# Kernel tuning notes

Measured on AMD Instinct MI355X. Metric: run time of the kernel, lower is better.

Reference implementation:

```python
import jax, jax.numpy as jnp
import numpy as np

EPS_DIST = 1e-10
BN_EPS = 1e-5
K = 3  # nsample / three_nn


def setup_inputs() -> dict:
    key = jax.random.key(0)
    ks = jax.random.split(key, 8)
    B, N, S, D1, D2 = 4, 8192, 2048, 128, 256
    C_in = D1 + D2  # 384
    H = 256
    inp = {
        "pos1": jax.random.normal(ks[0], (B, 3, N), dtype=jnp.float32),
        "pos2": jax.random.normal(ks[1], (B, 3, S), dtype=jnp.float32),
        "feature1": jax.random.normal(ks[2], (B, D1, N), dtype=jnp.float32),
        "feature2": jax.random.normal(ks[3], (B, D2, S), dtype=jnp.float32),
        # MLP layer 1: Conv1d(384->256, k=1) + BN
        "W1": jax.random.normal(ks[4], (H, C_in), dtype=jnp.float32) * (1.0 / np.sqrt(C_in)),
        "b1": jnp.zeros((H,), dtype=jnp.float32),
        "g1": jnp.ones((H,), dtype=jnp.float32),
        "be1": jnp.zeros((H,), dtype=jnp.float32),
        # MLP layer 2: Conv1d(256->256, k=1) + BN
        "W2": jax.random.normal(ks[5], (H, H), dtype=jnp.float32) * (1.0 / np.sqrt(H)),
        "b2": jnp.zeros((H,), dtype=jnp.float32),
        "g2": jnp.ones((H,), dtype=jnp.float32),
        "be2": jnp.zeros((H,), dtype=jnp.float32),
    }
    return inp


def _conv_bn_relu(x, W, b, gamma, beta):
    # x: [B, Cin, N]; 1x1 Conv1d == channel GEMM
    y = jnp.einsum("oc,bcn->bon", W, x) + b[None, :, None]
    # BatchNorm1d in training mode: batch statistics over (B, N)
    mean = jnp.mean(y, axis=(0, 2), keepdims=True)
    var = jnp.mean(jnp.square(y - mean), axis=(0, 2), keepdims=True)
    y = (y - mean) * jax.lax.rsqrt(var + BN_EPS)
    y = y * gamma[None, :, None] + beta[None, :, None]
    return jax.nn.relu(y)


def reference(pos1, pos2, feature1, feature2, W1, b1, g1, be1, W2, b2, g2, be2):
    # pos1: [B,3,N], pos2: [B,3,S], feature1: [B,D1,N], feature2: [B,D2,S]
    p1 = jnp.swapaxes(pos1, 1, 2)  # [B,N,3]
    p2 = jnp.swapaxes(pos2, 1, 2)  # [B,S,3]
    # three_nn: squared-distance 3-NN of each point in p1 among p2
    d2 = (jnp.sum(p1 * p1, -1)[:, :, None]
          + jnp.sum(p2 * p2, -1)[:, None, :]
          - 2.0 * jnp.einsum("bnc,bsc->bns", p1, p2))  # [B,N,S]
    neg_vals, idx = jax.lax.top_k(-d2, K)  # idx: [B,N,3]
    dists = jnp.maximum(-neg_vals, EPS_DIST)  # dists[dists<1e-10]=1e-10
    w = 1.0 / dists
    w = w / jnp.sum(w, -1, keepdims=True)  # [B,N,3]
    # grouping_operation: gather feature2 [B,D,S] by idx -> [B,D,N,3]
    grouped = jax.vmap(lambda f, i: f[:, i])(feature2, idx)
    interpolated = jnp.sum(grouped * w[:, None, :, :], axis=-1)  # [B,D2,N]
    feat = jnp.concatenate([interpolated, feature1], axis=1)  # [B,384,N]
    feat = _conv_bn_relu(feat, W1, b1, g1, be1)
    feat = _conv_bn_relu(feat, W2, b2, g2, be2)
    return feat  # [B,256,N]
```

## Files before the change

### kernel.cpp

```cpp
#include <hip/hip_runtime.h>
#include <hip/hip_bf16.h>
#include <cstdint>

typedef unsigned short u16;
typedef unsigned int u32;
typedef unsigned long long u64;
typedef __bf16 bf16x8 __attribute__((ext_vector_type(8)));
typedef float f32x4 __attribute__((ext_vector_type(4)));
typedef u16 u16x8 __attribute__((ext_vector_type(8)));

#define FPSCALE 1048576.0f
#define FPINV   (1.0f / 1048576.0f)
#define NSLICE 16

__device__ __forceinline__ u16 f2b(float f) {
    unsigned int u = __float_as_uint(f);
    u += 0x7fffu + ((u >> 16) & 1u);
    return (u16)(u >> 16);
}
__device__ __forceinline__ float b2f(u16 h) {
    return __uint_as_float(((unsigned int)h) << 16);
}
__device__ __forceinline__ void async_cp16(void* lds, const void* g) {
    __builtin_amdgcn_global_load_lds((const __attribute__((address_space(1))) void*)g,
                                     (__attribute__((address_space(3))) void*)lds, 16, 0, 0);
}
__device__ __forceinline__ u64 ld_agent_u64(const u64* p) {
    return __hip_atomic_load(p, __ATOMIC_RELAXED, __HIP_MEMORY_SCOPE_AGENT);
}
__device__ __forceinline__ u32 fmono(float f) {
    u32 u = __float_as_uint(f);
    return u ^ (((u32)((int)u >> 31)) | 0x80000000u);
}
__device__ __forceinline__ u64 shfl_xor_u64(u64 v, int mask) {
    u32 lo = (u32)v, hi = (u32)(v >> 32);
    lo = (u32)__shfl_xor((int)lo, mask);
    hi = (u32)__shfl_xor((int)hi, mask);
    return ((u64)hi << 32) | lo;
}
__device__ __forceinline__ void ins3(u64 k, u64& k0, u64& k1, u64& k2) {
    bool c0 = k > k0, c1 = k > k1, c2 = k > k2;
    k2 = c1 ? k1 : (c2 ? k : k2);
    k1 = c0 ? k0 : (c1 ? k : k1);
    k0 = c0 ? k : k0;
}
__device__ __forceinline__ int pkix(int i) { return i + (i >> 6); }

#define NB_NN  2048
#define NB_CVT 160
#define NB_T2  512
#define NB_T1  1024

__global__ __launch_bounds__(256, 8) void prep_kernel(const float* __restrict__ w1,
                                                      const float* __restrict__ w2,
                                                      u16* __restrict__ wb,
                                                      const float* __restrict__ feature2,
                                                      u16* __restrict__ f2t,
                                                      const float* __restrict__ feature1,
                                                      u16* __restrict__ f1t,
                                                      const float* __restrict__ pos1,
                                                      const float* __restrict__ pos2,
                                                      int* __restrict__ idx_out,
                                                      float* __restrict__ w_out,
                                                      u64* __restrict__ SZ) {
    __shared__ __align__(16) char smem[18176];
    int bi = blockIdx.x;
    int tid = threadIdx.x;

    if (bi >= NB_NN) {
        int ci = bi - NB_NN;
        if (ci >= NB_CVT + NB_T2 + NB_T1) {
            for (int i = tid; i < 2 * NSLICE * 512; i += 256) SZ[i] = 0;
            if (tid == 0) *(int*)(SZ + 2 * NSLICE * 512) = 0;
            return;
        }
        if (ci < NB_CVT) {
            int i = ci * 256 + tid;
            if (i < 40960) {
                const float* src = (i < 24576) ? w1 : w2;
                int k = (i < 24576) ? i : (i - 24576);
                float4 v = *(const float4*)&src[(size_t)k * 4];
                ushort4 o;
                o.x = f2b(v.x); o.y = f2b(v.y); o.z = f2b(v.z); o.w = f2b(v.w);
                *(ushort4*)&wb[(size_t)i * 4] = o;
            }
            return;
        }
        float (*t)[65] = (float (*)[65])smem;
        const float* in; u16* out; int C, S, s0, c0, b;
        if (ci < NB_CVT + NB_T2) {
            int lin = ci - NB_CVT;
            C = 256; S = 2048; in = feature2; out = f2t;
            s0 = (lin & 31) * 64; c0 = ((lin >> 5) & 3) * 64; b = lin >> 7;
        } else {
            int lin = ci - NB_CVT - NB_T2;
            C = 128; S = 8192; in = feature1; out = f1t;
            s0 = (lin & 127) * 64; c0 = ((lin >> 7) & 1) * 64; b = lin >> 8;
        }
        const float* ib = in + (size_t)b * C * S;
        u16* ob = out + (size_t)b * S * C;
        int col = tid & 63, r0 = tid >> 6;
#pragma unroll
        for (int p = 0; p < 16; ++p) {
            int c = p * 4 + r0;
            t[c][col] = ib[(size_t)(c0 + c) * S + s0 + col];
        }
        __syncthreads();
#pragma unroll
        for (int p = 0; p < 16; ++p) {
            int s = p * 4 + r0;
            ob[(size_t)(s0 + s) * C + c0 + col] = f2b(t[col][s]);
        }
        return;
    }

    float4* pk = (float4*)smem;
    u64* warr = (u64*)(smem + 16640);
    int j0 = bi * 16;
    int b = j0 >> 13;
    const float* p2 = pos2 + (size_t)b * 3 * 2048;
    int p = tid & 15, ck = tid >> 4;
    int wv = tid >> 6, lane = tid & 63;
    const float* p1 = pos1 + (size_t)b * 3 * 8192;
    int n = (j0 & 8191) + p;
    float qx = p1[n], qy = p1[8192 + n], qz = p1[16384 + n];
    u64 key0 = 0, key1 = 0, key2 = 0;

    for (int half = 0; half < 2; ++half) {
        int hbase = half * 1024;
        for (int i = tid; i < 1024; i += 256) {
            int s = hbase + i;
            float x = p2[s], y = p2[2048 + s], z = p2[4096 + s];
            pk[pkix(i)] = make_float4(x, y, z, -0.5f * (x * x + y * y + z * z));
        }
        __syncthreads();

        float g0 = -3.4e38f, g1 = -3.4e38f, g2 = -3.4e38f;
        int id0 = 0, id1 = 0, id2 = 0;
        int sb = ck * 64;
        const float4* pc = pk + pkix(sb);
#pragma unroll 4
        for (int it = 0; it < 64; ++it) {
            float4 cd = pc[it];
            int s = sb + it;
            float tv = fmaf(qx, cd.x, fmaf(qy, cd.y, fmaf(qz, cd.z, cd.w)));
            bool c0 = tv > g0, c1 = tv > g1, c2 = tv > g2;
            float o0 = g0, o1 = g1;
            g2 = __builtin_amdgcn_fmed3f(tv, o1, g2);
            g1 = __builtin_amdgcn_fmed3f(tv, o0, o1);
            g0 = fmaxf(o0, tv);
            id2 = c1 ? id1 : (c2 ? s : id2);
            id1 = c0 ? id0 : (c1 ? s : id1);
            id0 = c0 ? s : id0;
        }
        __syncthreads();

        ins3(((u64)fmono(g0) << 32) | (u64)(2047 - (hbase + id0)), key0, key1, key2);
        ins3(((u64)fmono(g1) << 32) | (u64)(2047 - (hbase + id1)), key0, key1, key2);
        ins3(((u64)fmono(g2) << 32) | (u64)(2047 - (hbase + id2)), key0, key1, key2);
    }

#pragma unroll
    for (int mask = 16; mask <= 32; mask <<= 1) {
        u64 m0 = shfl_xor_u64(key0, mask);
        u64 m1 = shfl_xor_u64(key1, mask);
        u64 m2 = shfl_xor_u64(key2, mask);
        ins3(m0, key0, key1, key2);
        ins3(m1, key0, key1, key2);
        ins3(m2, key0, key1, key2);
    }
    if (lane < 16) {
        u64* wr = &warr[(wv * 16 + p) * 3];
        wr[0] = key0; wr[1] = key1; wr[2] = key2;
    }
    __syncthreads();
    if (tid < 16) {
        int pp = tid;
        const u64* w0 = &warr[pp * 3];
        u64 k0 = w0[0], k1 = w0[1], k2 = w0[2];
#pragma unroll
        for (int w = 1; w < 4; ++w) {
            const u64* wr = &warr[(w * 16 + pp) * 3];
            ins3(wr[0], k0, k1, k2);
            ins3(wr[1], k0, k1, k2);
            ins3(wr[2], k0, k1, k2);
        }
        int s0 = 2047 - (int)(k0 & 0xFFFFFFFFu);
        int s1 = 2047 - (int)(k1 & 0xFFFFFFFFu);
        int s2 = 2047 - (int)(k2 & 0xFFFFFFFFu);
        int j = j0 + pp;
        int nn = j & 8191;
        float x1 = p1[nn], y1 = p1[8192 + nn], z1 = p1[16384 + nn];
        float n1 = x1 * x1 + y1 * y1 + z1 * z1;
        float X0 = p2[s0], Y0 = p2[2048 + s0], Z0 = p2[4096 + s0];
        float X1 = p2[s1], Y1v = p2[2048 + s1], Z1 = p2[4096 + s1];
        float X2 = p2[s2], Y2v = p2[2048 + s2], Z2 = p2[4096 + s2];
        float t0 = x1 * X0 + y1 * Y0 + z1 * Z0 - 0.5f * (X0 * X0 + Y0 * Y0 + Z0 * Z0);
        float t1 = x1 * X1 + y1 * Y1v + z1 * Z1 - 0.5f * (X1 * X1 + Y1v * Y1v + Z1 * Z1);
        float t2 = x1 * X2 + y1 * Y2v + z1 * Z2 - 0.5f * (X2 * X2 + Y2v * Y2v + Z2 * Z2);
        float d0 = fmaxf(fmaf(-2.f, t0, n1), 1e-10f);
        float d1 = fmaxf(fmaf(-2.f, t1, n1), 1e-10f);
        float d2 = fmaxf(fmaf(-2.f, t2, n1), 1e-10f);
        float w0v = 1.f / d0, w1v = 1.f / d1, w2v = 1.f / d2;
        float inv = 1.f / (w0v + w1v + w2v);
        idx_out[j * 3] = s0; idx_out[j * 3 + 1] = s1; idx_out[j * 3 + 2] = s2;
        w_out[j * 3] = w0v * inv; w_out[j * 3 + 1] = w1v * inv; w_out[j * 3 + 2] = w2v * inv;
    }
}

__global__ __launch_bounds__(256, 8) void interp_kernel(const u16* __restrict__ f2t,
                                                        const int* __restrict__ idx,
                                                        const float* __restrict__ wgt,
                                                        u16* __restrict__ out) {
    int tid = threadIdx.x;
    int j = blockIdx.x * 16 + (tid >> 4);
    int c0 = (tid & 15) * 16;
    int b = j >> 13;
    const u16* fb = f2t + (size_t)b * 2048 * 256;
    const u16* r0 = fb + (size_t)idx[j * 3 + 0] * 256 + c0;
    const u16* r1 = fb + (size_t)idx[j * 3 + 1] * 256 + c0;
    const u16* r2 = fb + (size_t)idx[j * 3 + 2] * 256 + c0;
    float w0 = wgt[j * 3 + 0], w1 = wgt[j * 3 + 1], w2 = wgt[j * 3 + 2];
    u16* ob = out + (size_t)j * 256 + c0;
#pragma unroll
    for (int cc = 0; cc < 2; ++cc) {
        u16x8 v0 = *(const u16x8*)(r0 + cc * 8);
        u16x8 v1 = *(const u16x8*)(r1 + cc * 8);
        u16x8 v2 = *(const u16x8*)(r2 + cc * 8);
        u16x8 o;
#pragma unroll
        for (int e = 0; e < 8; ++e)
            o[e] = f2b(w0 * b2f(v0[e]) + w1 * b2f(v1[e]) + w2 * b2f(v2[e]));
        *(u16x8*)(ob + cc * 8) = o;
    }
}

__device__ __forceinline__ void gridbar(int* cnt, int target) {
    __syncthreads();
    if (threadIdx.x == 0) {
        __hip_atomic_fetch_add(cnt, 1, __ATOMIC_RELAXED, __HIP_MEMORY_SCOPE_AGENT);
        while (__hip_atomic_load(cnt, __ATOMIC_RELAXED, __HIP_MEMORY_SCOPE_AGENT) < target)
            __builtin_amdgcn_s_sleep(16);
        __atomic_signal_fence(__ATOMIC_SEQ_CST);
    }
    __syncthreads();
}

__global__ __launch_bounds__(256, 1) void mlp_fused(const u16* __restrict__ A1,
                                                    const u16* __restrict__ A2g,
                                                    const u16* __restrict__ W1b,
                                                    const float* __restrict__ b1,
                                                    const u16* __restrict__ W2b,
                                                    const float* __restrict__ b2,
                                                    u64* __restrict__ S1,
                                                    const float* __restrict__ g1,
                                                    const float* __restrict__ be1,
                                                    u64* __restrict__ S2,
                                                    const float* __restrict__ g2,
                                                    const float* __restrict__ be2,
                                                    float* __restrict__ OUT,
                                                    int* __restrict__ BAR) {
    __shared__ __align__(16) char smem[98304];
    u16* AS  = (u16*)smem;
    u16* BS  = (u16*)(smem + 16384);
    u16* A2  = (u16*)smem;
    u16* BS2 = (u16*)(smem + 65536);
    float* SC  = (float*)(smem + 65536);
    float* SC2 = (float*)(smem + 65536 + 4096);
    float2* BNT = (float2*)(smem + 65536);

    int tid = threadIdx.x, bid = blockIdx.x;
    int lane = tid & 63, wv = tid >> 6;
    int l15 = lane & 15, q = lane >> 4;
    int lrow = lane >> 3, lchunk = lane & 7, schunk = lchunk ^ lrow;
    int j0 = bid * 128;
    int wrow = wv * 32;
    int sl = (bid & (NSLICE - 1)) * 512;

    f32x4 acc[2][16];
#pragma unroll
    for (int i = 0; i < 2; ++i)
#pragma unroll
        for (int jj = 0; jj < 16; ++jj) acc[i][jj] = (f32x4){0.f, 0.f, 0.f, 0.f};

    for (int k0 = 0; k0 < 384; k0 += 64) {
#pragma unroll
        for (int qq = 0; qq < 8; ++qq) {
            int row = wv * 64 + qq * 8;
            async_cp16(&BS[row * 64], W1b + (size_t)(row + lrow) * 384 + k0 + schunk * 8);
        }
        const u16* src; int str;
        if (k0 < 256) { src = A1 + (size_t)j0 * 256 + k0;          str = 256; }
        else          { src = A2g + (size_t)j0 * 128 + (k0 - 256); str = 128; }
#pragma unroll
        for (int qq = 0; qq < 4; ++qq) {
            int row = wv * 32 + qq * 8;
            async_cp16(&AS[row * 64], src + (size_t)(row + lrow) * str + schunk * 8);
        }
        __syncthreads();
#pragma unroll
        for (int ks = 0; ks < 2; ++ks) {
            bf16x8 af[2];
#pragma unroll
            for (int i = 0; i < 2; ++i) {
                int row = wrow + i * 16 + l15;
                af[i] = *(const bf16x8*)&AS[row * 64 + ((ks * 4 + q) ^ (l15 & 7)) * 8];
            }
#pragma unroll
            for (int jj = 0; jj < 16; ++jj) {
                int row = jj * 16 + l15;
                bf16x8 bfr = *(const bf16x8*)&BS[row * 64 + ((ks * 4 + q) ^ (l15 & 7)) * 8];
#pragma unroll
                for (int i = 0; i < 2; ++i)
                    acc[i][jj] = __builtin_amdgcn_mfma_f32_16x16x32_bf16(af[i], bfr,
                                                                         acc[i][jj], 0, 0, 0);
            }
        }
        __syncthreads();
    }

#pragma unroll
    for (int jj = 0; jj < 16; ++jj) {
        float bv = b1[jj * 16 + l15];
        float s = 0.f, s2 = 0.f;
#pragma unroll
        for (int i = 0; i < 2; ++i)
#pragma unroll
            for (int r = 0; r < 4; ++r) {
                acc[i][jj][r] += bv;
                float v = acc[i][jj][r];
                s += v; s2 += v * v;
            }
        s += __shfl_xor(s, 16); s += __shfl_xor(s, 32);
        s2 += __shfl_xor(s2, 16); s2 += __shfl_xor(s2, 32);
        if (q == 0) {
            SC[wv * 256 + jj * 16 + l15] = s;
            SC2[wv * 256 + jj * 16 + l15] = s2;
        }
    }
    __syncthreads();
    {
        float fs = SC[tid] + SC[256 + tid] + SC[512 + tid] + SC[768 + tid];
        float fs2 = SC2[tid] + SC2[256 + tid] + SC2[512 + tid] + SC2[768 + tid];
        atomicAdd(&S1[sl + tid], (u64)(long long)llrintf(fs * FPSCALE));
        atomicAdd(&S1[sl + 256 + tid], (u64)(long long)llrintf(fs2 * FPSCALE));
    }
    gridbar(BAR, 256);

    {
        long long su = 0, sq = 0;
#pragma unroll
        for (int r = 0; r < NSLICE; ++r) {
            su += (long long)ld_agent_u64(&S1[r * 512 + tid]);
            sq += (long long)ld_agent_u64(&S1[r * 512 + 256 + tid]);
        }
        float fs = (float)su * FPINV;
        float fs2 = (float)sq * FPINV;
        const float inv = 1.f / 32768.f;
        float mean = fs * inv;
        float var = fs2 * inv - mean * mean;
        float a = g1[tid] * rsqrtf(var + 1e-5f);
        BNT[tid] = make_float2(a, be1[tid] - mean * a);
    }
    __syncthreads();

#pragma unroll
    for (int i = 0; i < 2; ++i)
#pragma unroll
        for (int jj = 0; jj < 16; ++jj) {
            int c = jj * 16 + l15;
            float2 bn = BNT[c];
            int chunkbase = c >> 3;
            int win = c & 7;
#pragma unroll
            for (int r = 0; r < 4; ++r) {
                int row = wrow + i * 16 + q * 4 + r;
                float vb = b2f(f2b(acc[i][jj][r]));
                u16 h = f2b(fmaxf(vb * bn.x + bn.y, 0.f));
                A2[row * 256 + ((chunkbase ^ (row & 7)) * 8 + win)] = h;
            }
        }
    __syncthreads();

#pragma unroll
    for (int i = 0; i < 2; ++i)
#pragma unroll
        for (int jj = 0; jj < 16; ++jj) acc[i][jj] = (f32x4){0.f, 0.f, 0.f, 0.f};

    for (int kstep = 0; kstep < 4; ++kstep) {
        int k0 = kstep * 64;
#pragma unroll
        for (int qq = 0; qq < 8; ++qq) {
            int row = wv * 64 + qq * 8;
            async_cp16(&BS2[row * 64], W2b + (size_t)(row + lrow) * 256 + k0 + schunk * 8);
        }
        __syncthreads();
#pragma unroll
        for (int ks = 0; ks < 2; ++ks) {
            bf16x8 af[2];
#pragma unroll
            for (int i = 0; i < 2; ++i) {
                int row = wrow + i * 16 + l15;
                int kc = kstep * 8 + ks * 4 + q;
                af[i] = *(const bf16x8*)&A2[row * 256 + ((kc ^ (row & 7)) * 8)];
            }
#pragma unroll
            for (int jj = 0; jj < 16; ++jj) {
                int row = jj * 16 + l15;
                bf16x8 bfr = *(const bf16x8*)&BS2[row * 64 + ((ks * 4 + q) ^ (l15 & 7)) * 8];
#pragma unroll
                for (int i = 0; i < 2; ++i)
                    acc[i][jj] = __builtin_amdgcn_mfma_f32_16x16x32_bf16(af[i], bfr,
                                                                         acc[i][jj], 0, 0, 0);
            }
        }
        __syncthreads();
    }

#pragma unroll
    for (int jj = 0; jj < 16; ++jj) {
        float bv = b2[jj * 16 + l15];
        float s = 0.f, s2 = 0.f;
#pragma unroll
        for (int i = 0; i < 2; ++i)
#pragma unroll
            for (int r = 0; r < 4; ++r) {
                acc[i][jj][r] += bv;
                float v = acc[i][jj][r];
                s += v; s2 += v * v;
            }
        s += __shfl_xor(s, 16); s += __shfl_xor(s, 32);
        s2 += __shfl_xor(s2, 16); s2 += __shfl_xor(s2, 32);
        if (q == 0) {
            SC[wv * 256 + jj * 16 + l15] = s;
            SC2[wv * 256 + jj * 16 + l15] = s2;
        }
    }
    __syncthreads();
    {
        float fs = SC[tid] + SC[256 + tid] + SC[512 + tid] + SC[768 + tid];
        float fs2 = SC2[tid] + SC2[256 + tid] + SC2[512 + tid] + SC2[768 + tid];
        atomicAdd(&S2[sl + tid], (u64)(long long)llrintf(fs * FPSCALE));
        atomicAdd(&S2[sl + 256 + tid], (u64)(long long)llrintf(fs2 * FPSCALE));
    }
    gridbar(BAR, 512);

    {
        long long su = 0, sq = 0;
#pragma unroll
        for (int r = 0; r < NSLICE; ++r) {
            su += (long long)ld_agent_u64(&S2[r * 512 + tid]);
            sq += (long long)ld_agent_u64(&S2[r * 512 + 256 + tid]);
        }
        float fs = (float)su * FPINV;
        float fs2 = (float)sq * FPINV;
        const float inv = 1.f / 32768.f;
        float mean = fs * inv;
        float var = fs2 * inv - mean * mean;
        float a = g2[tid] * rsqrtf(var + 1e-5f);
        BNT[tid] = make_float2(a, be2[tid] - mean * a);
    }
    __syncthreads();

    int bb = j0 >> 13, nbase = j0 & 8191;
#pragma unroll
    for (int i = 0; i < 2; ++i)
#pragma unroll
        for (int jj = 0; jj < 16; ++jj) {
            int o = jj * 16 + l15;
            float2 bn = BNT[o];
            int n0 = nbase + wrow + i * 16 + q * 4;
            float4 v;
            v.x = fmaxf(b2f(f2b(acc[i][jj][0])) * bn.x + bn.y, 0.f);
            v.y = fmaxf(b2f(f2b(acc[i][jj][1])) * bn.x + bn.y, 0.f);
            v.z = fmaxf(b2f(f2b(acc[i][jj][2])) * bn.x + bn.y, 0.f);
            v.w = fmaxf(b2f(f2b(acc[i][jj][3])) * bn.x + bn.y, 0.f);
            *(float4*)&OUT[(size_t)bb * 2097152 + (size_t)o * 8192 + n0] = v;
        }
}

extern "C" void kernel_launch(void* const* d_in, const int* in_sizes, int n_in,
                              void* d_out, int out_size, void* d_ws, size_t ws_size,
                              hipStream_t stream) {
    const float* pos1 = (const float*)d_in[0];
    const float* pos2 = (const float*)d_in[1];
    const float* feature1 = (const float*)d_in[2];
    const float* feature2 = (const float*)d_in[3];
    const float* W1 = (const float*)d_in[4];
    const float* b1 = (const float*)d_in[5];
    const float* g1 = (const float*)d_in[6];
    const float* be1 = (const float*)d_in[7];
    const float* W2 = (const float*)d_in[8];
    const float* b2 = (const float*)d_in[9];
    const float* g2 = (const float*)d_in[10];
    const float* be2 = (const float*)d_in[11];

    char* ws = (char*)d_ws;
    int*    IDX   = (int*)(ws + 0);
    float*  WGT   = (float*)(ws + 393216);
    u16*    W1B   = (u16*)(ws + 786432);
    u16*    W2B   = (u16*)(ws + 983040);
    u16*    F2T   = (u16*)(ws + 1118208);
    u16*    F1T   = (u16*)(ws + 5312512);
    u16*    INTERP= (u16*)(ws + 30478336);
    u64*    SSTAT = (u64*)(ws + 47255552);
    u64*    S1    = SSTAT;
    u64*    S2    = SSTAT + NSLICE * 512;
    int*    BAR   = (int*)(SSTAT + 2 * NSLICE * 512);
    float*  OUT   = (float*)d_out;

    prep_kernel<<<NB_NN + NB_CVT + NB_T2 + NB_T1 + 1, 256, 0, stream>>>(
        W1, W2, W1B, feature2, F2T, feature1, F1T, pos1, pos2, IDX, WGT, SSTAT);
    interp_kernel<<<2048, 256, 0, stream>>>(F2T, IDX, WGT, INTERP);
    mlp_fused<<<256, 256, 0, stream>>>(INTERP, F1T, W1B, b1, W2B, b2,
                                       S1, g1, be1, S2, g2, be2, OUT, BAR);
}
```

Before: 183.2 us.

## Double-buffer MLP GEMM loads and split output channels across 8 waves

The fused MLP kernel now runs 512 threads per block, with waves split into 4 row groups and 2 column groups so each wave holds half as many accumulators. Both GEMM phases get double-buffered LDS staging, so the next K-slice of weights and activations is prefetched while the current one is computed. The first W2 slice is also prefetched before the BN1 grid barrier. The aim is to hide global-to-LDS latency and gain more latency hiding from extra waves per CU. The cost is more shared memory (about 138 KB) and a larger block.

```diff
diff --git a/kernel.cpp b/kernel.cpp
--- a/kernel.cpp
+++ b/kernel.cpp
@@ -246,7 +246,7 @@
     __syncthreads();
 }
 
-__global__ __launch_bounds__(256, 1) void mlp_fused(const u16* __restrict__ A1,
+__global__ __launch_bounds__(512, 1) void mlp_fused(const u16* __restrict__ A1,
                                                     const u16* __restrict__ A2g,
                                                     const u16* __restrict__ W1b,
                                                     const float* __restrict__ b1,
@@ -260,56 +260,79 @@
                                                     const float* __restrict__ be2,
                                                     float* __restrict__ OUT,
                                                     int* __restrict__ BAR) {
-    __shared__ __align__(16) char smem[98304];
+    __shared__ __align__(16) char smem[141312];
     u16* AS  = (u16*)smem;
-    u16* BS  = (u16*)(smem + 16384);
+    u16* BS  = (u16*)(smem + 32768);
     u16* A2  = (u16*)smem;
     u16* BS2 = (u16*)(smem + 65536);
-    float* SC  = (float*)(smem + 65536);
-    float* SC2 = (float*)(smem + 65536 + 4096);
-    float2* BNT = (float2*)(smem + 65536);
+    float* SC  = (float*)(smem + 131072);
+    float* SC2 = (float*)(smem + 135168);
+    float2* BNT = (float2*)(smem + 139264);
 
     int tid = threadIdx.x, bid = blockIdx.x;
     int lane = tid & 63, wv = tid >> 6;
     int l15 = lane & 15, q = lane >> 4;
     int lrow = lane >> 3, lchunk = lane & 7, schunk = lchunk ^ lrow;
     int j0 = bid * 128;
-    int wrow = wv * 32;
+    int rw = wv & 3;
+    int cg = wv >> 2;
+    int wrow = rw * 32;
+    int cbase = cg * 128;
     int sl = (bid & (NSLICE - 1)) * 512;
 
-    f32x4 acc[2][16];
+    f32x4 acc[2][8];
 #pragma unroll
     for (int i = 0; i < 2; ++i)
 #pragma unroll
-        for (int jj = 0; jj < 16; ++jj) acc[i][jj] = (f32x4){0.f, 0.f, 0.f, 0.f};
-
-    for (int k0 = 0; k0 < 384; k0 += 64) {
-#pragma unroll
-        for (int qq = 0; qq < 8; ++qq) {
-            int row = wv * 64 + qq * 8;
-            async_cp16(&BS[row * 64], W1b + (size_t)(row + lrow) * 384 + k0 + schunk * 8);
-        }
+        for (int jj = 0; jj < 8; ++jj) acc[i][jj] = (f32x4){0.f, 0.f, 0.f, 0.f};
+
+    auto stageB1 = [&](int buf, int k0) {
+#pragma unroll
+        for (int qq = 0; qq < 4; ++qq) {
+            int row = wv * 32 + qq * 8;
+            async_cp16(&BS[buf * 16384 + row * 64],
+                       W1b + (size_t)(row + lrow) * 384 + k0 + schunk * 8);
+        }
+    };
+    auto stageA1 = [&](int buf, int k0) {
         const u16* src; int str;
         if (k0 < 256) { src = A1 + (size_t)j0 * 256 + k0;          str = 256; }
         else          { src = A2g + (size_t)j0 * 128 + (k0 - 256); str = 128; }
 #pragma unroll
+        for (int qq = 0; qq < 2; ++qq) {
+            int row = wv * 16 + qq * 8;
+            async_cp16(&AS[buf * 8192 + row * 64],
+                       src + (size_t)(row + lrow) * str + schunk * 8);
+        }
+    };
+    auto stageB2 = [&](int buf, int k0) {
+#pragma unroll
         for (int qq = 0; qq < 4; ++qq) {
             int row = wv * 32 + qq * 8;
-            async_cp16(&AS[row * 64], src + (size_t)(row + lrow) * str + schunk * 8);
-        }
-        __syncthreads();
+            async_cp16(&BS2[buf * 16384 + row * 64],
+                       W2b + (size_t)(row + lrow) * 256 + k0 + schunk * 8);
+        }
+    };
+
+    stageB1(0, 0); stageA1(0, 0);
+    __syncthreads();
+    for (int t = 0; t < 6; ++t) {
+        int cur = t & 1;
+        if (t < 5) { stageB1(cur ^ 1, (t + 1) * 64); stageA1(cur ^ 1, (t + 1) * 64); }
 #pragma unroll
         for (int ks = 0; ks < 2; ++ks) {
             bf16x8 af[2];
 #pragma unroll
             for (int i = 0; i < 2; ++i) {
                 int row = wrow + i * 16 + l15;
-                af[i] = *(const bf16x8*)&AS[row * 64 + ((ks * 4 + q) ^ (l15 & 7)) * 8];
-            }
-#pragma unroll
-            for (int jj = 0; jj < 16; ++jj) {
-                int row = jj * 16 + l15;
-                bf16x8 bfr = *(const bf16x8*)&BS[row * 64 + ((ks * 4 + q) ^ (l15 & 7)) * 8];
+                af[i] = *(const bf16x8*)&AS[cur * 8192 + row * 64 +
+                                            ((ks * 4 + q) ^ (l15 & 7)) * 8];
+            }
+#pragma unroll
+            for (int jj = 0; jj < 8; ++jj) {
+                int brow = cbase + jj * 16 + l15;
+                bf16x8 bfr = *(const bf16x8*)&BS[cur * 16384 + brow * 64 +
+                                                 ((ks * 4 + q) ^ (l15 & 7)) * 8];
 #pragma unroll
                 for (int i = 0; i < 2; ++i)
                     acc[i][jj] = __builtin_amdgcn_mfma_f32_16x16x32_bf16(af[i], bfr,
@@ -319,9 +342,12 @@
         __syncthreads();
     }
 
-#pragma unroll
-    for (int jj = 0; jj < 16; ++jj) {
-        float bv = b1[jj * 16 + l15];
+    stageB2(0, 0);
+
+#pragma unroll
+    for (int jj = 0; jj < 8; ++jj) {
+        int c = cbase + jj * 16 + l15;
+        float bv = b1[c];
         float s = 0.f, s2 = 0.f;
 #pragma unroll
         for (int i = 0; i < 2; ++i)
@@ -333,13 +359,10 @@
             }
         s += __shfl_xor(s, 16); s += __shfl_xor(s, 32);
         s2 += __shfl_xor(s2, 16); s2 += __shfl_xor(s2, 32);
-        if (q == 0) {
-            SC[wv * 256 + jj * 16 + l15] = s;
-            SC2[wv * 256 + jj * 16 + l15] = s2;
-        }
-    }
-    __syncthreads();
-    {
+        if (q == 0) { SC[rw * 256 + c] = s; SC2[rw * 256 + c] = s2; }
+    }
+    __syncthreads();
+    if (tid < 256) {
         float fs = SC[tid] + SC[256 + tid] + SC[512 + tid] + SC[768 + tid];
         float fs2 = SC2[tid] + SC2[256 + tid] + SC2[512 + tid] + SC2[768 + tid];
         atomicAdd(&S1[sl + tid], (u64)(long long)llrintf(fs * FPSCALE));
@@ -347,7 +370,7 @@
     }
     gridbar(BAR, 256);
 
-    {
+    if (tid < 256) {
         long long su = 0, sq = 0;
 #pragma unroll
         for (int r = 0; r < NSLICE; ++r) {
@@ -365,13 +388,13 @@
     __syncthreads();
 
 #pragma unroll
-    for (int i = 0; i < 2; ++i)
-#pragma unroll
-        for (int jj = 0; jj < 16; ++jj) {
-            int c = jj * 16 + l15;
-            float2 bn = BNT[c];
-            int chunkbase = c >> 3;
-            int win = c & 7;
+    for (int jj = 0; jj < 8; ++jj) {
+        int c = cbase + jj * 16 + l15;
+        float2 bn = BNT[c];
+        int chunkbase = c >> 3;
+        int win = c & 7;
+#pragma unroll
+        for (int i = 0; i < 2; ++i)
 #pragma unroll
             for (int r = 0; r < 4; ++r) {
                 int row = wrow + i * 16 + q * 4 + r;
@@ -379,35 +402,31 @@
                 u16 h = f2b(fmaxf(vb * bn.x + bn.y, 0.f));
                 A2[row * 256 + ((chunkbase ^ (row & 7)) * 8 + win)] = h;
             }
-        }
+    }
     __syncthreads();
 
 #pragma unroll
     for (int i = 0; i < 2; ++i)
 #pragma unroll
-        for (int jj = 0; jj < 16; ++jj) acc[i][jj] = (f32x4){0.f, 0.f, 0.f, 0.f};
-
-    for (int kstep = 0; kstep < 4; ++kstep) {
-        int k0 = kstep * 64;
-#pragma unroll
-        for (int qq = 0; qq < 8; ++qq) {
-            int row = wv * 64 + qq * 8;
-            async_cp16(&BS2[row * 64], W2b + (size_t)(row + lrow) * 256 + k0 + schunk * 8);
-        }
-        __syncthreads();
+        for (int jj = 0; jj < 8; ++jj) acc[i][jj] = (f32x4){0.f, 0.f, 0.f, 0.f};
+
+    for (int t = 0; t < 4; ++t) {
+        int cur = t & 1;
+        if (t < 3) stageB2(cur ^ 1, (t + 1) * 64);
 #pragma unroll
         for (int ks = 0; ks < 2; ++ks) {
             bf16x8 af[2];
+            int kc = t * 8 + ks * 4 + q;
 #pragma unroll
             for (int i = 0; i < 2; ++i) {
                 int row = wrow + i * 16 + l15;
-                int kc = kstep * 8 + ks * 4 + q;
-                af[i] = *(const bf16x8*)&A2[row * 256 + ((kc ^ (row & 7)) * 8)];
-            }
-#pragma unroll
-            for (int jj = 0; jj < 16; ++jj) {
-                int row = jj * 16 + l15;
-                bf16x8 bfr = *(const bf16x8*)&BS2[row * 64 + ((ks * 4 + q) ^ (l15 & 7)) * 8];
+                af[i] = *(const bf16x8*)&A2[row * 256 + ((kc ^ (l15 & 7)) * 8)];
+            }
+#pragma unroll
+            for (int jj = 0; jj < 8; ++jj) {
+                int brow = cbase + jj * 16 + l15;
+                bf16x8 bfr = *(const bf16x8*)&BS2[cur * 16384 + brow * 64 +
+                                                  ((ks * 4 + q) ^ (l15 & 7)) * 8];
 #pragma unroll
                 for (int i = 0; i < 2; ++i)
                     acc[i][jj] = __builtin_amdgcn_mfma_f32_16x16x32_bf16(af[i], bfr,
@@ -418,8 +437,9 @@
     }
 
 #pragma unroll
-    for (int jj = 0; jj < 16; ++jj) {
-        float bv = b2[jj * 16 + l15];
+    for (int jj = 0; jj < 8; ++jj) {
+        int c = cbase + jj * 16 + l15;
+        float bv = b2[c];
         float s = 0.f, s2 = 0.f;
 #pragma unroll
         for (int i = 0; i < 2; ++i)
@@ -431,13 +451,10 @@
             }
         s += __shfl_xor(s, 16); s += __shfl_xor(s, 32);
         s2 += __shfl_xor(s2, 16); s2 += __shfl_xor(s2, 32);
-        if (q == 0) {
-            SC[wv * 256 + jj * 16 + l15] = s;
-            SC2[wv * 256 + jj * 16 + l15] = s2;
-        }
-    }
-    __syncthreads();
-    {
+        if (q == 0) { SC[rw * 256 + c] = s; SC2[rw * 256 + c] = s2; }
+    }
+    __syncthreads();
+    if (tid < 256) {
         float fs = SC[tid] + SC[256 + tid] + SC[512 + tid] + SC[768 + tid];
         float fs2 = SC2[tid] + SC2[256 + tid] + SC2[512 + tid] + SC2[768 + tid];
         atomicAdd(&S2[sl + tid], (u64)(long long)llrintf(fs * FPSCALE));
@@ -445,7 +462,7 @@
     }
     gridbar(BAR, 512);
 
-    {
+    if (tid < 256) {
         long long su = 0, sq = 0;
 #pragma unroll
         for (int r = 0; r < NSLICE; ++r) {
@@ -464,11 +481,11 @@
 
     int bb = j0 >> 13, nbase = j0 & 8191;
 #pragma unroll
-    for (int i = 0; i < 2; ++i)
-#pragma unroll
-        for (int jj = 0; jj < 16; ++jj) {
-            int o = jj * 16 + l15;
-            float2 bn = BNT[o];
+    for (int jj = 0; jj < 8; ++jj) {
+        int o = cbase + jj * 16 + l15;
+        float2 bn = BNT[o];
+#pragma unroll
+        for (int i = 0; i < 2; ++i) {
             int n0 = nbase + wrow + i * 16 + q * 4;
             float4 v;
             v.x = fmaxf(b2f(f2b(acc[i][jj][0])) * bn.x + bn.y, 0.f);
@@ -477,6 +494,7 @@
             v.w = fmaxf(b2f(f2b(acc[i][jj][3])) * bn.x + bn.y, 0.f);
             *(float4*)&OUT[(size_t)bb * 2097152 + (size_t)o * 8192 + n0] = v;
         }
+    }
 }
 
 extern "C" void kernel_launch(void* const* d_in, const int* in_sizes, int n_in,
@@ -512,6 +530,6 @@
     prep_kernel<<<NB_NN + NB_CVT + NB_T2 + NB_T1 + 1, 256, 0, stream>>>(
         W1, W2, W1B, feature2, F2T, feature1, F1T, pos1, pos2, IDX, WGT, SSTAT);
     interp_kernel<<<2048, 256, 0, stream>>>(F2T, IDX, WGT, INTERP);
-    mlp_fused<<<256, 256, 0, stream>>>(INTERP, F1T, W1B, b1, W2B, b2,
+    mlp_fused<<<256, 512, 0, stream>>>(INTERP, F1T, W1B, b1, W2B, b2,
                                        S1, g1, be1, S2, g2, be2, OUT, BAR);
 }
```

New measurement: 171.5 us. 1.07x faster.
